# Optimization experiments

Hardware: AMD Instinct MI355X
Metric: run time of the kernel (lower is better)

## Reference

```python
import jax, jax.numpy as jnp
import numpy as np

EPS = 1e-6
NHEADS = 16


def setup_inputs() -> dict:
    key = jax.random.key(0)
    ks = jax.random.split(key, 6)
    b, n, dim, h = 2, 2048, 2048, NHEADS
    d = dim // h
    x = jax.random.normal(ks[0], (b, n, dim), dtype=jnp.float32)
    qkv_w = jax.random.normal(ks[1], (3 * dim, dim), dtype=jnp.float32) * (dim ** -0.5)
    qkv_b = jax.random.normal(ks[2], (3 * dim,), dtype=jnp.float32) * 0.01
    q_norm_w = jnp.ones((d,), dtype=jnp.float32)
    k_norm_w = jnp.ones((d,), dtype=jnp.float32)
    # Flux-style rotation matrices: (1, 1, n, d/2, 2, 2)
    pos = jnp.arange(n, dtype=jnp.float32)[:, None]
    inv_freq = 1.0 / (10000.0 ** (jnp.arange(0, d, 2, dtype=jnp.float32) / d))  # [d/2]
    ang = pos * inv_freq[None, :]  # [n, d/2]
    cos, sin = jnp.cos(ang), jnp.sin(ang)
    rot = jnp.stack([jnp.stack([cos, -sin], axis=-1),
                     jnp.stack([sin, cos], axis=-1)], axis=-1)  # [n, d/2, 2, 2]
    rot = rot[None, None]  # [1,1,n,d/2,2,2]
    return {"x": x, "qkv_w": qkv_w, "qkv_b": qkv_b,
            "q_norm_w": q_norm_w, "k_norm_w": k_norm_w, "rot": rot}


def _rmsnorm(t, w):
    t32 = t.astype(jnp.float32)
    inv = jax.lax.rsqrt(jnp.mean(t32 * t32, axis=-1, keepdims=True) + EPS)
    return ((t32 * inv) * w).astype(t.dtype)


def _apply_rope(t, rot):
    # t: [b,h,n,d]; rot: [1,1,n,d/2,2,2]
    b, h, n, d = t.shape
    tx = t.astype(jnp.float32).reshape(b, h, n, d // 2, 1, 2)
    out = rot[..., 0] * tx[..., 0] + rot[..., 1] * tx[..., 1]  # [b,h,n,d/2,2]
    return out.reshape(b, h, n, d).astype(t.dtype)


def reference(x, qkv_w, qkv_b, q_norm_w, k_norm_w, rot):
    b, n, dim = x.shape
    d = q_norm_w.shape[0]
    h = dim // d
    qkv = x @ qkv_w.T + qkv_b  # [b, n, 3*dim]
    # layout per Rearrange 'b n (h d j) -> b h n d j'
    qkv = qkv.reshape(b, n, h, d, 3).transpose(0, 2, 1, 3, 4)  # [b,h,n,d,3]
    q, k, v = qkv[..., 0], qkv[..., 1], qkv[..., 2]
    q = _apply_rope(_rmsnorm(q, q_norm_w), rot)
    k = _apply_rope(_rmsnorm(k, k_norm_w), rot)
    scores = jnp.einsum('bhqd,bhkd->bhqk', q, k) * (d ** -0.5)
    attn = jax.nn.softmax(scores, axis=-1)
    out = jnp.einsum('bhqk,bhkd->bhqd', attn, v)
    return out.transpose(0, 2, 1, 3).reshape(b, n, dim)  # b n (h d)
```

## Files before the change

kernel.cpp:

```cpp
#include <hip/hip_runtime.h>
#include <cstdint>
#include <cstddef>


#define LOG2E 1.4426950408889634f
#define ATT_SCALE 0.08838834764831845f
#define QSCALE (ATT_SCALE * LOG2E)

typedef __attribute__((ext_vector_type(8))) __bf16 bf16x8;
typedef __attribute__((ext_vector_type(4))) __bf16 bf16x4;
typedef __attribute__((ext_vector_type(4))) float f32x4;

__device__ __forceinline__ float b2f(unsigned u) {
  u <<= 16;
  return __builtin_bit_cast(float, u);
}
__device__ __forceinline__ unsigned short f2b(float f) {
  unsigned x = __builtin_bit_cast(unsigned, f);
  return (unsigned short)((x + 0x7fffu + ((x >> 16) & 1u)) >> 16);
}
__device__ __forceinline__ void gl16(const void* g, void* l) {
  __builtin_amdgcn_global_load_lds((__attribute__((address_space(1))) void*)(g),
                                   (__attribute__((address_space(3))) void*)(l), 16, 0, 0);
}

__global__ void k_cvt(const float4* __restrict__ in, ushort4* __restrict__ out, int n4) {
  int i = blockIdx.x * blockDim.x + threadIdx.x;
  int st = gridDim.x * blockDim.x;
  for (; i < n4; i += st) {
    float4 v = in[i];
    ushort4 o;
    o.x = f2b(v.x); o.y = f2b(v.y); o.z = f2b(v.z); o.w = f2b(v.w);
    out[i] = o;
  }
}

__global__ __launch_bounds__(512, 2) void k_gemm(const unsigned short* __restrict__ A,
                                                 const unsigned short* __restrict__ W,
                                                 const float* __restrict__ bias,
                                                 unsigned short* __restrict__ C) {
  __shared__ __align__(16) unsigned short lds[65536];
  const int tid = threadIdx.x;
  const int w = tid >> 6, l = tid & 63;
  const int lo = l & 15, hi = l >> 4;
  const int WM = w >> 2, WN = w & 3;
  const int wg = blockIdx.x;
  const int swz = (wg & 7) * 48 + (wg >> 3);
  const int mbase = (swz / 24) * 256, nbase = (swz % 24) * 256;

  const int srow = w * 16 + (l >> 2);
  const int scol = ((l & 3) * 8) ^ ((srow & 3) << 3);

  auto stage_half = [&](int t, int rd) {
    unsigned short* Sa = lds + (t & 3) * 16384;
    unsigned short* Sb = Sa + 8192;
    const int kt = t * 32;
    gl16(A + (size_t)(mbase + rd * 128 + srow) * 2048 + kt + scol,
         Sa + (rd * 128 + w * 16) * 32);
    gl16(W + (size_t)(nbase + rd * 128 + srow) * 2048 + kt + scol,
         Sb + (rd * 128 + w * 16) * 32);
  };

  f32x4 acc[8][4] = {};
  stage_half(0, 0); stage_half(0, 1);
  stage_half(1, 0); stage_half(1, 1);
  stage_half(2, 0); stage_half(2, 1);

  const int ea = (hi * 8) ^ ((lo & 3) << 3);
  for (int t = 0; t < 64; ++t) {
    if (t < 62)       asm volatile("s_waitcnt vmcnt(8) lgkmcnt(0)" ::: "memory");
    else if (t == 62) asm volatile("s_waitcnt vmcnt(4) lgkmcnt(0)" ::: "memory");
    else              asm volatile("s_waitcnt vmcnt(0) lgkmcnt(0)" ::: "memory");
    __builtin_amdgcn_sched_barrier(0);
    __builtin_amdgcn_s_barrier();
    __builtin_amdgcn_sched_barrier(0);

    const unsigned short* Sa = lds + (t & 3) * 16384;
    const unsigned short* Sb = Sa + 8192;
    bf16x8 af[8], bf[4];

#pragma unroll
    for (int i = 0; i < 4; ++i)
      af[i] = *(const bf16x8*)&Sa[(WM * 128 + i * 16 + lo) * 32 + ea];
#pragma unroll
    for (int j = 0; j < 4; ++j)
      bf[j] = *(const bf16x8*)&Sb[(WN * 64 + j * 16 + lo) * 32 + ea];
    if (t + 3 < 64) stage_half(t + 3, 0);
    __builtin_amdgcn_sched_barrier(0);
    __builtin_amdgcn_s_barrier();
    __builtin_amdgcn_sched_barrier(0);
    __builtin_amdgcn_s_setprio(1);
#pragma unroll
    for (int i = 0; i < 4; ++i)
#pragma unroll
      for (int j = 0; j < 4; ++j)
        acc[i][j] = __builtin_amdgcn_mfma_f32_16x16x32_bf16(af[i], bf[j], acc[i][j], 0, 0, 0);
    __builtin_amdgcn_s_setprio(0);
    __builtin_amdgcn_sched_barrier(0);

#pragma unroll
    for (int i = 4; i < 8; ++i)
      af[i] = *(const bf16x8*)&Sa[(WM * 128 + i * 16 + lo) * 32 + ea];
    if (t + 3 < 64) stage_half(t + 3, 1);
    __builtin_amdgcn_sched_barrier(0);
    __builtin_amdgcn_s_barrier();
    __builtin_amdgcn_sched_barrier(0);
    __builtin_amdgcn_s_setprio(1);
#pragma unroll
    for (int i = 4; i < 8; ++i)
#pragma unroll
      for (int j = 0; j < 4; ++j)
        acc[i][j] = __builtin_amdgcn_mfma_f32_16x16x32_bf16(af[i], bf[j], acc[i][j], 0, 0, 0);
    __builtin_amdgcn_s_setprio(0);
    __builtin_amdgcn_sched_barrier(0);
  }

  const int rowb = mbase + WM * 128;
  const int colb = nbase + WN * 64;
#pragma unroll
  for (int j = 0; j < 4; ++j) {
    float bj = bias[colb + j * 16 + lo];
#pragma unroll
    for (int i = 0; i < 8; ++i)
#pragma unroll
      for (int r = 0; r < 4; ++r) {
        int row = rowb + i * 16 + hi * 4 + r;
        C[(size_t)row * 6144 + colb + j * 16 + lo] = f2b(acc[i][j][r] + bj);
      }
  }
}

__global__ __launch_bounds__(256) void k_normrope(const unsigned short* __restrict__ qkv,
                                                  const float* __restrict__ qw,
                                                  const float* __restrict__ kw,
                                                  const float* __restrict__ rot,
                                                  unsigned short* __restrict__ Q,
                                                  unsigned short* __restrict__ K,
                                                  unsigned short* __restrict__ V) {
  const int l = threadIdx.x & 63;
  const int idx = blockIdx.x * 4 + (threadIdx.x >> 6);
  const int h = idx & 15;
  const int n = (idx >> 4) & 2047;
  const int b = idx >> 15;
  const unsigned* p = (const unsigned*)(qkv + (size_t)(b * 2048 + n) * 6144 + h * 384 + l * 6);
  unsigned u0 = p[0], u1 = p[1], u2 = p[2];
  float q0 = b2f(u0 & 0xffff), k0 = b2f(u0 >> 16);
  float v0 = b2f(u1 & 0xffff), q1 = b2f(u1 >> 16);
  float k1 = b2f(u2 & 0xffff), v1 = b2f(u2 >> 16);
  (void)v0; (void)v1;
  float sq = q0 * q0 + q1 * q1, sk = k0 * k0 + k1 * k1;
#pragma unroll
  for (int m = 1; m < 64; m <<= 1) {
    sq += __shfl_xor(sq, m, 64);
    sk += __shfl_xor(sk, m, 64);
  }
  float qi = rsqrtf(sq * (1.0f / 128.0f) + 1e-6f) * QSCALE;
  float ki = rsqrtf(sk * (1.0f / 128.0f) + 1e-6f);
  float2 qwv = *(const float2*)&qw[2 * l];
  float2 kwv = *(const float2*)&kw[2 * l];
  float4 r = *(const float4*)&rot[n * 256 + l * 4];
  float qn0 = q0 * qi * qwv.x, qn1 = q1 * qi * qwv.y;
  float kn0 = k0 * ki * kwv.x, kn1 = k1 * ki * kwv.y;
  unsigned qo = (unsigned)f2b(r.x * qn0 + r.y * qn1) | ((unsigned)f2b(r.z * qn0 + r.w * qn1) << 16);
  unsigned ko = (unsigned)f2b(r.x * kn0 + r.y * kn1) | ((unsigned)f2b(r.z * kn0 + r.w * kn1) << 16);
  unsigned vo = (u1 & 0xffffu) | (u2 & 0xffff0000u);
  size_t ob = ((size_t)(b * 16 + h) * 2048 + n) * 128 + 2 * l;
  *(unsigned*)(Q + ob) = qo;
  *(unsigned*)(K + ob) = ko;
  *(unsigned*)(V + ob) = vo;
}

__global__ __launch_bounds__(256) void k_transpose(const unsigned short* __restrict__ V,
                                                   unsigned short* __restrict__ Vt) {
  __shared__ unsigned short tile[64 * 66];
  const int t = threadIdx.x;
  const int d0 = blockIdx.x * 64;
  const int n0 = blockIdx.y * 64;
  const int bh = blockIdx.z;
#pragma unroll
  for (int s = t; s < 512; s += 256) {
    int nr = s >> 3, c8 = (s & 7) * 8;
    uint4 vv = *(const uint4*)(V + ((size_t)bh * 2048 + n0 + nr) * 128 + d0 + c8);
    unsigned* tp = (unsigned*)&tile[nr * 66 + c8];
    tp[0] = vv.x; tp[1] = vv.y; tp[2] = vv.z; tp[3] = vv.w;
  }
  __syncthreads();
#pragma unroll
  for (int s = t; s < 512; s += 256) {
    int dr = s >> 3, n8 = (s & 7) * 8;
    unsigned short e[8];
#pragma unroll
    for (int j = 0; j < 8; ++j) e[j] = tile[(n8 + j) * 66 + dr];
    uint4 o;
    o.x = e[0] | ((unsigned)e[1] << 16);
    o.y = e[2] | ((unsigned)e[3] << 16);
    o.z = e[4] | ((unsigned)e[5] << 16);
    o.w = e[6] | ((unsigned)e[7] << 16);
    *(uint4*)(Vt + ((size_t)bh * 128 + d0 + dr) * 2048 + n0 + n8) = o;
  }
}

__global__ __launch_bounds__(512, 4) void k_attn(const unsigned short* __restrict__ Q,
                                                 const unsigned short* __restrict__ K,
                                                 const unsigned short* __restrict__ Vt,
                                                 float* __restrict__ out) {
  __shared__ __align__(16) unsigned short lds[40960];
  unsigned short* Ps = lds + 32768;
  const int tid = threadIdx.x;
  const int w = tid >> 6, l = tid & 63;
  const int lo = l & 15, hi = l >> 4;
  const int swz = (lo & 7) << 3;
  const int qt = blockIdx.x, bh = blockIdx.y;
  const unsigned short* Qb = Q + (size_t)bh * 2048 * 128;
  const unsigned short* Kb = K + (size_t)bh * 2048 * 128;
  const unsigned short* Vb = Vt + (size_t)bh * 128 * 2048;
  unsigned short* Psw = Ps + w * 1024;

  bf16x8 qf[4];
  const int qrow = qt * 128 + w * 16 + lo;
#pragma unroll
  for (int dk = 0; dk < 4; ++dk)
    qf[dk] = *(const bf16x8*)&Qb[(size_t)qrow * 128 + dk * 32 + hi * 8];

  f32x4 Oacc[8] = {};
  float m_run = -__builtin_inff(), l_run = 0.0f;

  const int krow0 = w * 4 + hi;
  const int vrow0 = w * 8 + (l >> 3);
  const unsigned short* kp = Kb + (size_t)krow0 * 128 + ((lo * 8) ^ ((krow0 & 7) << 3));
  const unsigned short* vp = Vb + (size_t)vrow0 * 2048 + (((l & 7) * 8) ^ ((vrow0 & 7) << 3));

  auto stage = [&](int t, int b) {
    unsigned short* Ksb = lds + b * 16384;
    unsigned short* Vtsb = Ksb + 8192;
#pragma unroll
    for (int r = 0; r < 2; ++r) {
      gl16(kp + (size_t)t * 8192 + r * 4096,
           Ksb + (r * 32 + w * 4) * 128);
      gl16(vp + (size_t)r * 131072 + t * 64,
           Vtsb + (r * 64 + w * 8) * 64);
    }
  };

  stage(0, 0);
  int cur = 0;
  for (int t = 0; t < 32; ++t) {
    __syncthreads();
    if (t + 1 < 32) stage(t + 1, cur ^ 1);
    const unsigned short* Ks = lds + cur * 16384;
    const unsigned short* Vts = Ks + 8192;

    f32x4 S[4] = {};
#pragma unroll
    for (int kf = 0; kf < 4; ++kf)
#pragma unroll
      for (int dk = 0; dk < 4; ++dk)
        S[kf] = __builtin_amdgcn_mfma_f32_16x16x32_bf16(
            *(const bf16x8*)&Ks[(kf * 16 + lo) * 128 + ((dk * 32 + hi * 8) ^ swz)],
            qf[dk], S[kf], 0, 0, 0);

    float m01, m23, mt;
    m01 = fmaxf(fmaxf(S[0][0], S[0][1]), fmaxf(S[0][2], S[0][3]));
    m23 = fmaxf(fmaxf(S[1][0], S[1][1]), fmaxf(S[1][2], S[1][3]));
    mt = fmaxf(m01, m23);
    m01 = fmaxf(fmaxf(S[2][0], S[2][1]), fmaxf(S[2][2], S[2][3]));
    m23 = fmaxf(fmaxf(S[3][0], S[3][1]), fmaxf(S[3][2], S[3][3]));
    mt = fmaxf(mt, fmaxf(m01, m23));
    mt = fmaxf(mt, __shfl_xor(mt, 16, 64));
    mt = fmaxf(mt, __shfl_xor(mt, 32, 64));

    const bool defer = __all(mt <= m_run + 8.0f);
    float m_new = m_run, alpha = 1.0f;
    if (!defer) {
      m_new = fmaxf(m_run, mt);
      alpha = exp2f(m_run - m_new);
    }

    float p[4][4];
    float ls = 0.0f;
#pragma unroll
    for (int kf = 0; kf < 4; ++kf)
#pragma unroll
      for (int r = 0; r < 4; ++r) {
        p[kf][r] = exp2f(S[kf][r] - m_new);
        ls += p[kf][r];
      }
    ls += __shfl_xor(ls, 16, 64);
    ls += __shfl_xor(ls, 32, 64);

#pragma unroll
    for (int kf = 0; kf < 4; ++kf) {
      bf16x4 pk;
      pk[0] = (__bf16)p[kf][0]; pk[1] = (__bf16)p[kf][1];
      pk[2] = (__bf16)p[kf][2]; pk[3] = (__bf16)p[kf][3];
      *(bf16x4*)&Psw[lo * 64 + ((kf * 16 + hi * 4) ^ swz)] = pk;
    }

    if (!defer) {
#pragma unroll
      for (int df = 0; df < 8; ++df) {
        Oacc[df][0] *= alpha; Oacc[df][1] *= alpha;
        Oacc[df][2] *= alpha; Oacc[df][3] *= alpha;
      }
      l_run = l_run * alpha + ls;
      m_run = m_new;
    } else {
      l_run += ls;
    }

    const bf16x8 pb0 = *(const bf16x8*)&Psw[lo * 64 + ((hi * 8) ^ swz)];
    const bf16x8 pb1 = *(const bf16x8*)&Psw[lo * 64 + ((32 + hi * 8) ^ swz)];
#pragma unroll
    for (int df = 0; df < 8; ++df) {
      Oacc[df] = __builtin_amdgcn_mfma_f32_16x16x32_bf16(
          *(const bf16x8*)&Vts[(df * 16 + lo) * 64 + ((hi * 8) ^ swz)], pb0, Oacc[df], 0, 0, 0);
      Oacc[df] = __builtin_amdgcn_mfma_f32_16x16x32_bf16(
          *(const bf16x8*)&Vts[(df * 16 + lo) * 64 + ((32 + hi * 8) ^ swz)], pb1, Oacc[df], 0, 0, 0);
    }
    cur ^= 1;
  }

  const float inv = 1.0f / l_run;
  __syncthreads();
  float* Ot = ((float*)lds) + w * 2048;
#pragma unroll
  for (int df = 0; df < 8; ++df)
#pragma unroll
    for (int r = 0; r < 4; ++r)
      Ot[lo * 128 + df * 16 + hi * 4 + r] = Oacc[df][r] * inv;
  const int b = bh >> 4, h = bh & 15;
  const int q2 = l >> 2, c = (l & 3) * 32;
  float* op = out + ((size_t)(b * 2048 + qt * 128 + w * 16 + q2) * 2048 + h * 128 + c);
#pragma unroll
  for (int u = 0; u < 8; ++u)
    *(float4*)&op[u * 4] = *(const float4*)&Ot[q2 * 128 + c + u * 4];
}

extern "C" void kernel_launch(void* const* d_in, const int* in_sizes, int n_in,
                              void* d_out, int out_size, void* d_ws, size_t ws_size,
                              hipStream_t stream) {
  (void)in_sizes; (void)n_in; (void)out_size; (void)ws_size;
  const float* x = (const float*)d_in[0];
  const float* qkv_w = (const float*)d_in[1];
  const float* qkv_b = (const float*)d_in[2];
  const float* q_norm_w = (const float*)d_in[3];
  const float* k_norm_w = (const float*)d_in[4];
  const float* rot = (const float*)d_in[5];
  float* out = (float*)d_out;
  char* ws = (char*)d_ws;
  unsigned short* xb  = (unsigned short*)(ws);
  unsigned short* wb  = (unsigned short*)(ws + 16777216);
  unsigned short* qkv = (unsigned short*)(ws + 41943040);
  unsigned short* Qb  = (unsigned short*)(ws + 92274688);
  unsigned short* Kb  = (unsigned short*)(ws + 109051904);
  unsigned short* Vb  = (unsigned short*)(ws + 125829120);
  unsigned short* Vtb = (unsigned short*)(ws);

  hipLaunchKernelGGL(k_cvt, dim3(1024), dim3(256), 0, stream,
                     (const float4*)x, (ushort4*)xb, 8388608 / 4);
  hipLaunchKernelGGL(k_cvt, dim3(1024), dim3(256), 0, stream,
                     (const float4*)qkv_w, (ushort4*)wb, 12582912 / 4);
  hipLaunchKernelGGL(k_gemm, dim3(384), dim3(512), 0, stream, xb, wb, qkv_b, qkv);
  hipLaunchKernelGGL(k_normrope, dim3(16384), dim3(256), 0, stream,
                     qkv, q_norm_w, k_norm_w, rot, Qb, Kb, Vb);
  hipLaunchKernelGGL(k_transpose, dim3(2, 32, 32), dim3(256), 0, stream, Vb, Vtb);
  hipLaunchKernelGGL(k_attn, dim3(16, 32), dim3(512), 0, stream, Qb, Kb, Vtb, out);
}
```

Baseline: 278.9 us.

## Switch QKV GEMM to double-buffered LDS with doubled occupancy target

Result: slower. 1.109 ms (+297.4%).

```diff
diff --git a/kernel.cpp b/kernel.cpp
--- a/kernel.cpp
+++ b/kernel.cpp
@@ -35,11 +35,11 @@
   }
 }
 
-__global__ __launch_bounds__(512, 2) void k_gemm(const unsigned short* __restrict__ A,
+__global__ __launch_bounds__(512, 4) void k_gemm(const unsigned short* __restrict__ A,
                                                  const unsigned short* __restrict__ W,
                                                  const float* __restrict__ bias,
                                                  unsigned short* __restrict__ C) {
-  __shared__ __align__(16) unsigned short lds[65536];
+  __shared__ __align__(16) unsigned short lds[32768];
   const int tid = threadIdx.x;
   const int w = tid >> 6, l = tid & 63;
   const int lo = l & 15, hi = l >> 4;
@@ -49,70 +49,53 @@
   const int mbase = (swz / 24) * 256, nbase = (swz % 24) * 256;
 
   const int srow = w * 16 + (l >> 2);
-  const int scol = ((l & 3) * 8) ^ ((srow & 3) << 3);
-
-  auto stage_half = [&](int t, int rd) {
-    unsigned short* Sa = lds + (t & 3) * 16384;
+  const int scol = ((l & 3) * 8) ^ (((srow >> 1) & 3) << 3);
+
+  auto stage = [&](int t, int buf) {
+    unsigned short* Sa = lds + buf * 16384;
     unsigned short* Sb = Sa + 8192;
     const int kt = t * 32;
-    gl16(A + (size_t)(mbase + rd * 128 + srow) * 2048 + kt + scol,
-         Sa + (rd * 128 + w * 16) * 32);
-    gl16(W + (size_t)(nbase + rd * 128 + srow) * 2048 + kt + scol,
-         Sb + (rd * 128 + w * 16) * 32);
+#pragma unroll
+    for (int rd = 0; rd < 2; ++rd) {
+      gl16(A + (size_t)(mbase + rd * 128 + srow) * 2048 + kt + scol,
+           Sa + (rd * 128 + w * 16) * 32);
+      gl16(W + (size_t)(nbase + rd * 128 + srow) * 2048 + kt + scol,
+           Sb + (rd * 128 + w * 16) * 32);
+    }
   };
 
   f32x4 acc[8][4] = {};
-  stage_half(0, 0); stage_half(0, 1);
-  stage_half(1, 0); stage_half(1, 1);
-  stage_half(2, 0); stage_half(2, 1);
-
-  const int ea = (hi * 8) ^ ((lo & 3) << 3);
+  stage(0, 0);
+
+  const int ea = (hi * 8) ^ (((lo >> 1) & 3) << 3);
   for (int t = 0; t < 64; ++t) {
-    if (t < 62)       asm volatile("s_waitcnt vmcnt(8) lgkmcnt(0)" ::: "memory");
-    else if (t == 62) asm volatile("s_waitcnt vmcnt(4) lgkmcnt(0)" ::: "memory");
-    else              asm volatile("s_waitcnt vmcnt(0) lgkmcnt(0)" ::: "memory");
+    asm volatile("s_waitcnt vmcnt(0) lgkmcnt(0)" ::: "memory");
     __builtin_amdgcn_sched_barrier(0);
     __builtin_amdgcn_s_barrier();
     __builtin_amdgcn_sched_barrier(0);
-
-    const unsigned short* Sa = lds + (t & 3) * 16384;
+    const int cur = t & 1;
+    if (t + 1 < 64) stage(t + 1, cur ^ 1);
+
+    const unsigned short* Sa = lds + cur * 16384;
     const unsigned short* Sb = Sa + 8192;
     bf16x8 af[8], bf[4];
-
 #pragma unroll
     for (int i = 0; i < 4; ++i)
       af[i] = *(const bf16x8*)&Sa[(WM * 128 + i * 16 + lo) * 32 + ea];
 #pragma unroll
     for (int j = 0; j < 4; ++j)
       bf[j] = *(const bf16x8*)&Sb[(WN * 64 + j * 16 + lo) * 32 + ea];
-    if (t + 3 < 64) stage_half(t + 3, 0);
-    __builtin_amdgcn_sched_barrier(0);
-    __builtin_amdgcn_s_barrier();
-    __builtin_amdgcn_sched_barrier(0);
+#pragma unroll
+    for (int i = 4; i < 8; ++i)
+      af[i] = *(const bf16x8*)&Sa[(WM * 128 + i * 16 + lo) * 32 + ea];
+
     __builtin_amdgcn_s_setprio(1);
 #pragma unroll
-    for (int i = 0; i < 4; ++i)
+    for (int i = 0; i < 8; ++i)
 #pragma unroll
       for (int j = 0; j < 4; ++j)
         acc[i][j] = __builtin_amdgcn_mfma_f32_16x16x32_bf16(af[i], bf[j], acc[i][j], 0, 0, 0);
     __builtin_amdgcn_s_setprio(0);
-    __builtin_amdgcn_sched_barrier(0);
-
-#pragma unroll
-    for (int i = 4; i < 8; ++i)
-      af[i] = *(const bf16x8*)&Sa[(WM * 128 + i * 16 + lo) * 32 + ea];
-    if (t + 3 < 64) stage_half(t + 3, 1);
-    __builtin_amdgcn_sched_barrier(0);
-    __builtin_amdgcn_s_barrier();
-    __builtin_amdgcn_sched_barrier(0);
-    __builtin_amdgcn_s_setprio(1);
-#pragma unroll
-    for (int i = 4; i < 8; ++i)
-#pragma unroll
-      for (int j = 0; j < 4; ++j)
-        acc[i][j] = __builtin_amdgcn_mfma_f32_16x16x32_bf16(af[i], bf[j], acc[i][j], 0, 0, 0);
-    __builtin_amdgcn_s_setprio(0);
-    __builtin_amdgcn_sched_barrier(0);
   }
 
   const int rowb = mbase + WM * 128;
```
